# Kernel tuning notes

Hardware: AMD Instinct MI355X
Metric: run time of the kernel (lower is better)

Reference implementation:

```python
import jax, jax.numpy as jnp
import numpy as np

EMBED_DIM = 2048
NUM_HEADS = 16
LATENT_DIM = 512
HEAD_DIM = EMBED_DIM // NUM_HEADS


def setup_inputs() -> dict:
    key = jax.random.key(0)
    ks = jax.random.split(key, 9)
    s = 0.02
    x = jax.random.normal(ks[0], (2, 2048, EMBED_DIM), dtype=jnp.float32)
    # torch Linear weights stored as [out, in]
    q_w = jax.random.normal(ks[1], (EMBED_DIM, EMBED_DIM), jnp.float32) * s
    q_b = jax.random.normal(ks[2], (EMBED_DIM,), jnp.float32) * s
    kvd_w = jax.random.normal(ks[3], (LATENT_DIM, EMBED_DIM), jnp.float32) * s
    kvd_b = jax.random.normal(ks[4], (LATENT_DIM,), jnp.float32) * s
    kvu_w = jax.random.normal(ks[5], (EMBED_DIM * 2, LATENT_DIM), jnp.float32) * s
    kvu_b = jax.random.normal(ks[6], (EMBED_DIM * 2,), jnp.float32) * s
    out_w = jax.random.normal(ks[7], (EMBED_DIM, EMBED_DIM), jnp.float32) * s
    out_b = jax.random.normal(ks[8], (EMBED_DIM,), jnp.float32) * s
    return {"x": x, "q_w": q_w, "q_b": q_b, "kvd_w": kvd_w, "kvd_b": kvd_b,
            "kvu_w": kvu_w, "kvu_b": kvu_b, "out_w": out_w, "out_b": out_b}


def reference(x, q_w, q_b, kvd_w, kvd_b, kvu_w, kvu_b, out_w, out_b):
    b, s, _ = x.shape
    q = x @ q_w.T + q_b                      # [b,s,E]
    latent = x @ kvd_w.T + kvd_b             # [b,s,L]
    kv = latent @ kvu_w.T + kvu_b            # [b,s,2E]
    k, v = kv[..., :EMBED_DIM], kv[..., EMBED_DIM:]
    def heads(t):
        return t.reshape(b, s, NUM_HEADS, HEAD_DIM).transpose(0, 2, 1, 3)  # [b,h,s,d]
    qh, kh, vh = heads(q), heads(k), heads(v)
    scores = jnp.einsum('bhqd,bhkd->bhqk', qh, kh) / jnp.sqrt(jnp.float32(HEAD_DIM))
    attn = jax.nn.softmax(scores, axis=-1)
    out = jnp.einsum('bhqk,bhkd->bhqd', attn, vh)
    out = out.transpose(0, 2, 1, 3).reshape(b, s, EMBED_DIM)
    return out @ out_w.T + out_b
```

## Files before the change

kernel.cpp:

```cpp
#include <hip/hip_runtime.h>

typedef unsigned short u16;
typedef __attribute__((ext_vector_type(8))) __bf16 bf16x8;
typedef __attribute__((ext_vector_type(8))) unsigned short u16x8;
typedef __attribute__((ext_vector_type(4))) float f32x4;
typedef __attribute__((ext_vector_type(16))) float f32x16;

#define BK 32
#define TILE_ELEMS (128 * BK)

__device__ __forceinline__ u16 f32_to_bf16(float f) {
  unsigned int u = __builtin_bit_cast(unsigned int, f);
  u += 0x7fffu + ((u >> 16) & 1u);
  return (u16)(u >> 16);
}

__global__ __launch_bounds__(256) void cvt_bf16(const float* __restrict__ in,
                                                u16* __restrict__ out, int n) {
  int i = (blockIdx.x * 256 + threadIdx.x) * 4;
  if (i >= n) return;
  float4 v = *(const float4*)(in + i);
  ushort4 o;
  o.x = f32_to_bf16(v.x);
  o.y = f32_to_bf16(v.y);
  o.z = f32_to_bf16(v.z);
  o.w = f32_to_bf16(v.w);
  *(ushort4*)(out + i) = o;
}

__device__ __forceinline__ void gemm_core(const u16* __restrict__ A_tile,
                                          const u16* __restrict__ B_tile, int K,
                                          u16* As, u16* Bs, f32x4 acc[4][4]) {
  const int tid = threadIdx.x;
  const int w = tid >> 6, lane = tid & 63;
  const int wm = (w >> 1) << 6, wn = (w & 1) << 6;
  const int quad = lane >> 4, l15 = lane & 15;

  const u16* Ap = A_tile + (tid >> 2) * K + (tid & 3) * 8;
  const u16* Bp = B_tile + (tid >> 2) * K + (tid & 3) * 8;

  u16x8 ra0 = *(const u16x8*)Ap;
  u16x8 ra1 = *(const u16x8*)(Ap + 64 * K);
  u16x8 rb0 = *(const u16x8*)Bp;
  u16x8 rb1 = *(const u16x8*)(Bp + 64 * K);
  *(u16x8*)(As + tid * 8) = ra0;
  *(u16x8*)(As + (256 + tid) * 8) = ra1;
  *(u16x8*)(Bs + tid * 8) = rb0;
  *(u16x8*)(Bs + (256 + tid) * 8) = rb1;

  int p = 0;
  for (int k0 = 0; k0 < K; k0 += BK) {
    const int kn = (k0 + BK < K) ? (k0 + BK) : 0;
    ra0 = *(const u16x8*)(Ap + kn);
    ra1 = *(const u16x8*)(Ap + 64 * K + kn);
    rb0 = *(const u16x8*)(Bp + kn);
    rb1 = *(const u16x8*)(Bp + 64 * K + kn);
    __syncthreads();
    const u16* Asr = As + p * TILE_ELEMS;
    const u16* Bsr = Bs + p * TILE_ELEMS;
    bf16x8 af[4], bf[4];
#pragma unroll
    for (int i = 0; i < 4; i++)
      af[i] = *(const bf16x8*)(Asr + (wm + i * 16 + l15) * BK + quad * 8);
#pragma unroll
    for (int j = 0; j < 4; j++)
      bf[j] = *(const bf16x8*)(Bsr + (wn + j * 16 + l15) * BK + quad * 8);
#pragma unroll
    for (int i = 0; i < 4; i++)
#pragma unroll
      for (int j = 0; j < 4; j++)
        acc[i][j] =
            __builtin_amdgcn_mfma_f32_16x16x32_bf16(af[i], bf[j], acc[i][j], 0, 0, 0);
    const int pn = p ^ 1;
    u16* Asw = As + pn * TILE_ELEMS;
    u16* Bsw = Bs + pn * TILE_ELEMS;
    *(u16x8*)(Asw + tid * 8) = ra0;
    *(u16x8*)(Asw + (256 + tid) * 8) = ra1;
    *(u16x8*)(Bsw + tid * 8) = rb0;
    *(u16x8*)(Bsw + (256 + tid) * 8) = rb1;
    p = pn;
  }
}

__global__ __launch_bounds__(256) void gemm_qlat(const u16* __restrict__ X,
                                                 const u16* __restrict__ QW,
                                                 const u16* __restrict__ KVDW,
                                                 const float* __restrict__ q_b,
                                                 const float* __restrict__ kvd_b,
                                                 u16* __restrict__ Qb,
                                                 u16* __restrict__ Lat) {
  __shared__ __align__(16) u16 As[2 * TILE_ELEMS];
  __shared__ __align__(16) u16 Bs[2 * TILE_ELEMS];
  const int bn = blockIdx.x, bm = blockIdx.y;
  const bool isq = bn < 16;
  const u16* B_tile = isq ? QW + (size_t)bn * 128 * 2048
                          : KVDW + (size_t)(bn - 16) * 128 * 2048;
  f32x4 acc[4][4];
  const f32x4 z = {0.f, 0.f, 0.f, 0.f};
#pragma unroll
  for (int i = 0; i < 4; i++)
#pragma unroll
    for (int j = 0; j < 4; j++) acc[i][j] = z;
  gemm_core(X + (size_t)bm * 128 * 2048, B_tile, 2048, As, Bs, acc);

  const float* bias = isq ? q_b : kvd_b;
  u16* C = isq ? Qb : Lat;
  const int N = isq ? 2048 : 512;
  const int colbase = (isq ? bn : bn - 16) * 128;

  const int tid = threadIdx.x;
  const int w = tid >> 6, lane = tid & 63;
  const int wm = (w >> 1) << 6, wn = (w & 1) << 6;
  const int quad = lane >> 4, l15 = lane & 15;
  const int row0 = bm * 128 + wm + quad * 4;
  const int col0 = colbase + wn + l15;
#pragma unroll
  for (int i = 0; i < 4; i++)
#pragma unroll
    for (int j = 0; j < 4; j++) {
      int col = col0 + j * 16;
      float bv = bias[col];
#pragma unroll
      for (int r = 0; r < 4; r++) {
        int row = row0 + i * 16 + r;
        C[(size_t)row * N + col] = f32_to_bf16(acc[i][j][r] + bv);
      }
    }
}

__global__ __launch_bounds__(256) void gemm_f32out(const u16* __restrict__ A,
                                                   const u16* __restrict__ B,
                                                   const float* __restrict__ bias,
                                                   float* __restrict__ C, int K, int N) {
  __shared__ __align__(16) u16 As[2 * TILE_ELEMS];
  __shared__ __align__(16) u16 Bs[2 * TILE_ELEMS];
  f32x4 acc[4][4];
  const f32x4 z = {0.f, 0.f, 0.f, 0.f};
#pragma unroll
  for (int i = 0; i < 4; i++)
#pragma unroll
    for (int j = 0; j < 4; j++) acc[i][j] = z;
  gemm_core(A + (size_t)blockIdx.y * 128 * K, B + (size_t)blockIdx.x * 128 * K, K,
            As, Bs, acc);

  const int tid = threadIdx.x;
  const int w = tid >> 6, lane = tid & 63;
  const int wm = (w >> 1) << 6, wn = (w & 1) << 6;
  const int quad = lane >> 4, l15 = lane & 15;
  const int row0 = blockIdx.y * 128 + wm + quad * 4;
  const int col0 = blockIdx.x * 128 + wn + l15;
#pragma unroll
  for (int i = 0; i < 4; i++)
#pragma unroll
    for (int j = 0; j < 4; j++) {
      int col = col0 + j * 16;
      float bv = bias[col];
#pragma unroll
      for (int r = 0; r < 4; r++) {
        int row = row0 + i * 16 + r;
        C[(size_t)row * N + col] = acc[i][j][r] + bv;
      }
    }
}

__global__ __launch_bounds__(256) void gemm_kv(const u16* __restrict__ A,
                                               const u16* __restrict__ B,
                                               const float* __restrict__ bias,
                                               u16* __restrict__ Khat,
                                               u16* __restrict__ Vt, int K) {
  __shared__ __align__(16) u16 As[2 * TILE_ELEMS];
  __shared__ __align__(16) u16 Bs[2 * TILE_ELEMS];
  f32x4 acc[4][4];
  const f32x4 z = {0.f, 0.f, 0.f, 0.f};
#pragma unroll
  for (int i = 0; i < 4; i++)
#pragma unroll
    for (int j = 0; j < 4; j++) acc[i][j] = z;
  gemm_core(A + (size_t)blockIdx.y * 128 * K, B + (size_t)blockIdx.x * 128 * K, K,
            As, Bs, acc);

  const int tid = threadIdx.x;
  const int w = tid >> 6, lane = tid & 63;
  const int wm = (w >> 1) << 6, wn = (w & 1) << 6;
  const int quad = lane >> 4, l15 = lane & 15;
  const int row0 = blockIdx.y * 128 + wm + quad * 4;
  const int col0 = blockIdx.x * 128 + wn + l15;
#pragma unroll
  for (int i = 0; i < 4; i++)
#pragma unroll
    for (int j = 0; j < 4; j++) {
      int n = col0 + j * 16;
      float bv = bias[n];
#pragma unroll
      for (int r = 0; r < 4; r++) {
        int row = row0 + i * 16 + r;
        int bb = row >> 11, s = row & 2047;
        u16 val = f32_to_bf16(acc[i][j][r] + bv);
        if (n < 2048) {
          int h = n >> 7, d = n & 127;
          Khat[((size_t)(bb * 16 + h) * 2048 + s) * 128 + d] = val;
        } else {
          int h = (n - 2048) >> 7, d = n & 127;
          Vt[((size_t)(bb * 16 + h) * 128 + d) * 2048 + s] = val;
        }
      }
    }
}

__global__ __launch_bounds__(256) void attn_kernel(const u16* __restrict__ Q,
                                                   const u16* __restrict__ Khat,
                                                   const u16* __restrict__ Vt,
                                                   u16* __restrict__ O) {
  __shared__ __align__(16) u16 Ks[64 * 136];
  __shared__ __align__(16) u16 Vs[128 * 72];
  __shared__ __align__(16) u16 Ps[4 * 32 * 72];

  const int tid = threadIdx.x;
  const int w = tid >> 6, lane = tid & 63;
  const int l31 = lane & 31, half = lane >> 5;
  const int qt = blockIdx.x & 15;
  const int h = (blockIdx.x >> 4) & 15;
  const int b = blockIdx.x >> 8;
  const int bh = b * 16 + h;
  const float SC = 0.08838834764831845f * 1.4426950408889634f;

  bf16x8 qf[8];
  {
    const u16* qrow = Q + (size_t)(b * 2048 + qt * 128 + w * 32 + l31) * 2048 +
                      h * 128 + half * 8;
#pragma unroll
    for (int kc = 0; kc < 8; kc++) qf[kc] = *(const bf16x8*)(qrow + kc * 16);
  }

  f32x16 oacc[4];
#pragma unroll
  for (int nt = 0; nt < 4; nt++)
#pragma unroll
    for (int r = 0; r < 16; r++) oacc[nt][r] = 0.f;
  float lsum[16];
#pragma unroll
  for (int r = 0; r < 16; r++) lsum[r] = 0.f;

  const u16* Kg = Khat + (size_t)bh * 2048 * 128;
  const u16* Vg = Vt + (size_t)bh * 128 * 2048;
  u16* Pw = Ps + w * 32 * 72;

  for (int key0 = 0; key0 < 2048; key0 += 64) {
    u16x8 kv[4], vv[4];
#pragma unroll
    for (int it = 0; it < 4; it++) {
      int slot = it * 256 + tid;
      int kr = slot >> 4, c = slot & 15;
      kv[it] = *(const u16x8*)(Kg + (size_t)(key0 + kr) * 128 + c * 8);
    }
#pragma unroll
    for (int it = 0; it < 4; it++) {
      int slot = it * 256 + tid;
      int d = slot >> 3, c = slot & 7;
      vv[it] = *(const u16x8*)(Vg + (size_t)d * 2048 + key0 + c * 8);
    }
    __syncthreads();
#pragma unroll
    for (int it = 0; it < 4; it++) {
      int slot = it * 256 + tid;
      int kr = slot >> 4, c = slot & 15;
      *(u16x8*)(Ks + kr * 136 + c * 8) = kv[it];
    }
#pragma unroll
    for (int it = 0; it < 4; it++) {
      int slot = it * 256 + tid;
      int d = slot >> 3, c = slot & 7;
      *(u16x8*)(Vs + d * 72 + c * 8) = vv[it];
    }
    __syncthreads();

    f32x16 sacc[2];
#pragma unroll
    for (int ct = 0; ct < 2; ct++)
#pragma unroll
      for (int r = 0; r < 16; r++) sacc[ct][r] = 0.f;
#pragma unroll
    for (int ct = 0; ct < 2; ct++)
#pragma unroll
      for (int kc = 0; kc < 8; kc++) {
        bf16x8 kf =
            *(const bf16x8*)(Ks + (ct * 32 + l31) * 136 + kc * 16 + half * 8);
        sacc[ct] =
            __builtin_amdgcn_mfma_f32_32x32x16_bf16(qf[kc], kf, sacc[ct], 0, 0, 0);
      }

#pragma unroll
    for (int ct = 0; ct < 2; ct++)
#pragma unroll
      for (int r = 0; r < 16; r++) {
        float e = exp2f(sacc[ct][r] * SC);
        lsum[r] += e;
        int ridx = (r & 3) + 8 * (r >> 2) + 4 * half;
        Pw[ridx * 72 + ct * 32 + l31] = f32_to_bf16(e);
      }

    bf16x8 pf[4];
#pragma unroll
    for (int kc = 0; kc < 4; kc++)
      pf[kc] = *(const bf16x8*)(Pw + l31 * 72 + kc * 16 + half * 8);
#pragma unroll
    for (int nt = 0; nt < 4; nt++)
#pragma unroll
      for (int kc = 0; kc < 4; kc++) {
        bf16x8 vf =
            *(const bf16x8*)(Vs + (nt * 32 + l31) * 72 + kc * 16 + half * 8);
        oacc[nt] =
            __builtin_amdgcn_mfma_f32_32x32x16_bf16(pf[kc], vf, oacc[nt], 0, 0, 0);
      }
  }

#pragma unroll
  for (int r = 0; r < 16; r++) {
    float s = lsum[r];
    s += __shfl_xor(s, 1);
    s += __shfl_xor(s, 2);
    s += __shfl_xor(s, 4);
    s += __shfl_xor(s, 8);
    s += __shfl_xor(s, 16);
    lsum[r] = 1.0f / s;
  }

#pragma unroll
  for (int nt = 0; nt < 4; nt++)
#pragma unroll
    for (int r = 0; r < 16; r++) {
      int ridx = (r & 3) + 8 * (r >> 2) + 4 * half;
      int row = b * 2048 + qt * 128 + w * 32 + ridx;
      int col = h * 128 + nt * 32 + l31;
      O[(size_t)row * 2048 + col] = f32_to_bf16(oacc[nt][r] * lsum[r]);
    }
}

extern "C" void kernel_launch(void* const* d_in, const int* in_sizes, int n_in,
                              void* d_out, int out_size, void* d_ws, size_t ws_size,
                              hipStream_t stream) {
  (void)in_sizes; (void)n_in; (void)out_size; (void)ws_size;
  const float* x     = (const float*)d_in[0];
  const float* q_w   = (const float*)d_in[1];
  const float* q_b   = (const float*)d_in[2];
  const float* kvd_w = (const float*)d_in[3];
  const float* kvd_b = (const float*)d_in[4];
  const float* kvu_w = (const float*)d_in[5];
  const float* kvu_b = (const float*)d_in[6];
  const float* out_w = (const float*)d_in[7];
  const float* out_b = (const float*)d_in[8];
  float* out = (float*)d_out;

  char* p = (char*)d_ws;
  u16* X    = (u16*)(p + 0);
  u16* W1   = (u16*)(p + (size_t)16 * 1024 * 1024);
  u16* W2   = (u16*)(p + (size_t)24 * 1024 * 1024);
  u16* Qb   = (u16*)(p + (size_t)26 * 1024 * 1024);
  u16* Lat  = (u16*)(p + (size_t)42 * 1024 * 1024);
  u16* Khat = (u16*)(p + (size_t)46 * 1024 * 1024);
  u16* Vt   = (u16*)(p + (size_t)62 * 1024 * 1024);
  u16* AO   = (u16*)(p + (size_t)78 * 1024 * 1024);

  cvt_bf16<<<dim3(8192), dim3(256), 0, stream>>>(x, X, 8388608);
  cvt_bf16<<<dim3(4096), dim3(256), 0, stream>>>(q_w, W1, 4194304);
  cvt_bf16<<<dim3(1024), dim3(256), 0, stream>>>(kvd_w, W2, 1048576);

  gemm_qlat<<<dim3(20, 32), dim3(256), 0, stream>>>(X, W1, W2, q_b, kvd_b, Qb, Lat);

  cvt_bf16<<<dim3(2048), dim3(256), 0, stream>>>(kvu_w, W1, 2097152);
  gemm_kv<<<dim3(32, 32), dim3(256), 0, stream>>>(Lat, W1, kvu_b, Khat, Vt, 512);

  cvt_bf16<<<dim3(4096), dim3(256), 0, stream>>>(out_w, X, 4194304);
  attn_kernel<<<dim3(512), dim3(256), 0, stream>>>(Qb, Khat, Vt, AO);
  gemm_f32out<<<dim3(16, 32), dim3(256), 0, stream>>>(AO, X, out_b, out, 2048, 2048);
}
```

Before: 411.4 us.

## Double-buffer K/V tiles in attention and shrink key tile to 32

Restructures the attention loop to use double-buffered shared-memory tiles for K and V. The next tile's global loads are issued before the current tile's MFMA work and stored to the alternate buffer afterwards, leaving one barrier per iteration instead of two. The key tile shrinks from 64 to 32 keys, halving per-iteration register staging and LDS footprint but doubling the iteration count. The last iteration wastefully prefetches tile 0 again.

```diff
diff --git a/kernel.cpp b/kernel.cpp
--- a/kernel.cpp
+++ b/kernel.cpp
@@ -211,9 +211,9 @@
                                                    const u16* __restrict__ Khat,
                                                    const u16* __restrict__ Vt,
                                                    u16* __restrict__ O) {
-  __shared__ __align__(16) u16 Ks[64 * 136];
-  __shared__ __align__(16) u16 Vs[128 * 72];
-  __shared__ __align__(16) u16 Ps[4 * 32 * 72];
+  __shared__ __align__(16) u16 Ks[2][32 * 136];
+  __shared__ __align__(16) u16 Vs[2][128 * 40];
+  __shared__ __align__(16) u16 Ps[4 * 32 * 40];
 
   const int tid = threadIdx.x;
   const int w = tid >> 6, lane = tid & 63;
@@ -243,75 +243,69 @@
 
   const u16* Kg = Khat + (size_t)bh * 2048 * 128;
   const u16* Vg = Vt + (size_t)bh * 128 * 2048;
-  u16* Pw = Ps + w * 32 * 72;
-
-  for (int key0 = 0; key0 < 2048; key0 += 64) {
-    u16x8 kv[4], vv[4];
-#pragma unroll
-    for (int it = 0; it < 4; it++) {
-      int slot = it * 256 + tid;
-      int kr = slot >> 4, c = slot & 15;
-      kv[it] = *(const u16x8*)(Kg + (size_t)(key0 + kr) * 128 + c * 8);
-    }
-#pragma unroll
-    for (int it = 0; it < 4; it++) {
-      int slot = it * 256 + tid;
-      int d = slot >> 3, c = slot & 7;
-      vv[it] = *(const u16x8*)(Vg + (size_t)d * 2048 + key0 + c * 8);
+  u16* Pw = Ps + w * 32 * 40;
+
+  const int kkr = tid >> 4, kc0 = tid & 15;
+  const int vd = tid >> 2, vc0 = tid & 3;
+
+  u16x8 kv[2], vv[2];
+#pragma unroll
+  for (int it = 0; it < 2; it++) {
+    kv[it] = *(const u16x8*)(Kg + (size_t)(kkr + it * 16) * 128 + kc0 * 8);
+    vv[it] = *(const u16x8*)(Vg + (size_t)(vd + it * 64) * 2048 + vc0 * 8);
+  }
+#pragma unroll
+  for (int it = 0; it < 2; it++) {
+    *(u16x8*)(Ks[0] + (kkr + it * 16) * 136 + kc0 * 8) = kv[it];
+    *(u16x8*)(Vs[0] + (vd + it * 64) * 40 + vc0 * 8) = vv[it];
+  }
+
+  int p = 0;
+  for (int key0 = 0; key0 < 2048; key0 += 32) {
+    const int kn = (key0 + 32 < 2048) ? (key0 + 32) : 0;
+#pragma unroll
+    for (int it = 0; it < 2; it++) {
+      kv[it] = *(const u16x8*)(Kg + (size_t)(kn + kkr + it * 16) * 128 + kc0 * 8);
+      vv[it] = *(const u16x8*)(Vg + (size_t)(vd + it * 64) * 2048 + kn + vc0 * 8);
     }
     __syncthreads();
-#pragma unroll
-    for (int it = 0; it < 4; it++) {
-      int slot = it * 256 + tid;
-      int kr = slot >> 4, c = slot & 15;
-      *(u16x8*)(Ks + kr * 136 + c * 8) = kv[it];
-    }
-#pragma unroll
-    for (int it = 0; it < 4; it++) {
-      int slot = it * 256 + tid;
-      int d = slot >> 3, c = slot & 7;
-      *(u16x8*)(Vs + d * 72 + c * 8) = vv[it];
-    }
-    __syncthreads();
-
-    f32x16 sacc[2];
-#pragma unroll
-    for (int ct = 0; ct < 2; ct++)
-#pragma unroll
-      for (int r = 0; r < 16; r++) sacc[ct][r] = 0.f;
-#pragma unroll
-    for (int ct = 0; ct < 2; ct++)
-#pragma unroll
-      for (int kc = 0; kc < 8; kc++) {
-        bf16x8 kf =
-            *(const bf16x8*)(Ks + (ct * 32 + l31) * 136 + kc * 16 + half * 8);
-        sacc[ct] =
-            __builtin_amdgcn_mfma_f32_32x32x16_bf16(qf[kc], kf, sacc[ct], 0, 0, 0);
+
+    f32x16 sacc;
+#pragma unroll
+    for (int r = 0; r < 16; r++) sacc[r] = 0.f;
+#pragma unroll
+    for (int kc = 0; kc < 8; kc++) {
+      bf16x8 kf = *(const bf16x8*)(Ks[p] + l31 * 136 + kc * 16 + half * 8);
+      sacc = __builtin_amdgcn_mfma_f32_32x32x16_bf16(qf[kc], kf, sacc, 0, 0, 0);
+    }
+
+#pragma unroll
+    for (int r = 0; r < 16; r++) {
+      float e = exp2f(sacc[r] * SC);
+      lsum[r] += e;
+      int ridx = (r & 3) + 8 * (r >> 2) + 4 * half;
+      Pw[ridx * 40 + l31] = f32_to_bf16(e);
+    }
+
+    bf16x8 pf[2];
+#pragma unroll
+    for (int kc = 0; kc < 2; kc++)
+      pf[kc] = *(const bf16x8*)(Pw + l31 * 40 + kc * 16 + half * 8);
+#pragma unroll
+    for (int nt = 0; nt < 4; nt++)
+#pragma unroll
+      for (int kc = 0; kc < 2; kc++) {
+        bf16x8 vf = *(const bf16x8*)(Vs[p] + (nt * 32 + l31) * 40 + kc * 16 + half * 8);
+        oacc[nt] = __builtin_amdgcn_mfma_f32_32x32x16_bf16(pf[kc], vf, oacc[nt], 0, 0, 0);
       }
 
-#pragma unroll
-    for (int ct = 0; ct < 2; ct++)
-#pragma unroll
-      for (int r = 0; r < 16; r++) {
-        float e = exp2f(sacc[ct][r] * SC);
-        lsum[r] += e;
-        int ridx = (r & 3) + 8 * (r >> 2) + 4 * half;
-        Pw[ridx * 72 + ct * 32 + l31] = f32_to_bf16(e);
-      }
-
-    bf16x8 pf[4];
-#pragma unroll
-    for (int kc = 0; kc < 4; kc++)
-      pf[kc] = *(const bf16x8*)(Pw + l31 * 72 + kc * 16 + half * 8);
-#pragma unroll
-    for (int nt = 0; nt < 4; nt++)
-#pragma unroll
-      for (int kc = 0; kc < 4; kc++) {
-        bf16x8 vf =
-            *(const bf16x8*)(Vs + (nt * 32 + l31) * 72 + kc * 16 + half * 8);
-        oacc[nt] =
-            __builtin_amdgcn_mfma_f32_32x32x16_bf16(pf[kc], vf, oacc[nt], 0, 0, 0);
-      }
+    const int pn = p ^ 1;
+#pragma unroll
+    for (int it = 0; it < 2; it++) {
+      *(u16x8*)(Ks[pn] + (kkr + it * 16) * 136 + kc0 * 8) = kv[it];
+      *(u16x8*)(Vs[pn] + (vd + it * 64) * 40 + vc0 * 8) = vv[it];
+    }
+    p = pn;
   }
 
 #pragma unroll
```

Measured after the change: 415.7 us. No clear change (+1.0%).
